# Optimization experiments

Hardware: AMD Instinct MI355X
Metric: run time of the kernel (lower is better)

## Reference

```python
import jax, jax.numpy as jnp
import numpy as np

B, D, N, M, R, C = 512, 16, 64, 32, 32, 10  # batch, divisions, feat_in, feat_map, TR-rank, categories


def setup_inputs() -> dict:
    key = jax.random.key(0)
    k1, k2, k3, k4 = jax.random.split(key, 4)
    tensor = jax.random.normal(k1, (B, D, N), dtype=jnp.float32)
    W_fm = jax.random.normal(k2, (N, M), dtype=jnp.float32) / np.sqrt(N)
    b_fm = jax.random.normal(k3, (M,), dtype=jnp.float32) * 0.01
    # one [R, M, R] tensor-ring core per (category, division)
    G = jax.random.normal(k4, (C, D, R, M, R), dtype=jnp.float32) / np.sqrt(M * R)
    return {"tensor": tensor, "W_fm": W_fm, "b_fm": b_fm, "G": G}


def reference(tensor, W_fm, b_fm, G):
    # FeatureMap: learned linear n -> m applied per division  [B, D, M]
    feat = jnp.einsum('bdn,nm->bdm', tensor, W_fm) + b_fm
    # CoreKernelTensorRing per (category, division): [B,M] x [R,M,R] -> [B,R,R]
    cores = jnp.einsum('bdm,cdimj->cdbij', feat, G)  # [C, D, B, R, R]
    # __foward_products: chained batched matmul along divisions (structural loop, D fixed)
    prod = cores[:, 0]  # [C, B, R, R]
    for d in range(1, D):
        prod = jnp.matmul(prod, cores[:, d])
    # __calculate_traces: per-sample trace, one logit per category
    logits = jnp.einsum('cbii->bc', prod)  # [B, C]
    return jax.nn.log_softmax(logits, axis=1)
```

## Files before the change

kernel.cpp:

```cpp
#include <hip/hip_runtime.h>
#include <math.h>

#define BB 512
#define DD 16
#define NN 64
#define MM 32
#define RR 32
#define CC 10
#define BBLK 16
#define ROWH 40
#define BREGH 1304

typedef _Float16 v8h __attribute__((ext_vector_type(8)));
typedef float v4f __attribute__((ext_vector_type(4)));

union H8 { unsigned int u[4]; v8h h; _Float16 e[8]; };
union H4 { unsigned int u[2]; _Float16 e[4]; };

__global__ __launch_bounds__(256) void produce_kernel(
    const float* __restrict__ tensor, const float* __restrict__ W,
    const float* __restrict__ bias,   const float* __restrict__ G,
    _Float16* __restrict__ fh,        _Float16* __restrict__ gh) {
    __shared__ __align__(16) char smem[36864];
    const int t = threadIdx.x;
    if (blockIdx.x < 1024) {
        float* ten_s = (float*)smem;
        float* W_s   = (float*)smem + 512;
        const int bd0 = blockIdx.x * 8;
        if (t < 128)
            *(float4*)(ten_s + t * 4) = *(const float4*)(tensor + bd0 * NN + t * 4);
        *(float4*)(W_s + t * 4)        = *(const float4*)(W + t * 4);
        *(float4*)(W_s + 1024 + t * 4) = *(const float4*)(W + 1024 + t * 4);
        __syncthreads();
        const int m = t & 31, bd_l = t >> 5;
        float acc = bias[m];
#pragma unroll
        for (int n = 0; n < NN; ++n) acc += ten_s[bd_l * NN + n] * W_s[n * MM + m];
        fh[(bd0 + bd_l) * MM + m] = (_Float16)acc;
    } else {
        _Float16* lg = (_Float16*)smem;
        const int pb = blockIdx.x - 1024;
        const int c  = pb >> 5;
        const int d  = (pb >> 1) & 15;
        const int hf = pb & 1;
        const float* src = G + (size_t)(c * DD + d) * 32768 + hf * 16384;
#pragma unroll
        for (int k = 0; k < 16; ++k) {
            const int f = (k * 256 + t) * 4;
            float4 v = *(const float4*)(src + f);
            const int di = f >> 10, m = (f >> 5) & 31, j = f & 31;
            H4 hv;
            hv.e[0] = (_Float16)v.x; hv.e[1] = (_Float16)v.y;
            hv.e[2] = (_Float16)v.z; hv.e[3] = (_Float16)v.w;
            *(uint2*)(lg + di * 1152 + m * 36 + j) = make_uint2(hv.u[0], hv.u[1]);
        }
        __syncthreads();
#pragma unroll
        for (int k = 0; k < 8; ++k) {
            const int idx = k * 256 + t;
            const int tl = idx >> 6, ln = idx & 63;
            const int di = tl >> 1, jh = tl & 1;
            const int q = ln >> 4, j4 = ln & 15;
            const int j = jh * 16 + j4;
            H8 o;
#pragma unroll
            for (int r = 0; r < 8; ++r)
                o.e[r] = lg[di * 1152 + (8 * q + r) * 36 + j];
            const size_t gi = ((size_t)(c * DD + d) * 64 + hf * 32 + tl) * 64 + ln;
            *(v8h*)(gh + gi * 8) = o.h;
        }
    }
}

__global__ __launch_bounds__(512, 4) void chain_kernel(
    const _Float16* __restrict__ feat_h,
    const _Float16* __restrict__ g_h,
    float* __restrict__ trout)
{
    __shared__ __align__(16) _Float16 lds[BBLK * BREGH];

    const int bid = blockIdx.x;
    const int xcd = bid & 7;
    const int idx = bid >> 3;
    int c, sub;
    if (idx < 32) { c = xcd; sub = idx; }
    else {
        const int e = idx - 32;
        if (xcd >= 2 && xcd <= 5) { c = 8; sub = (xcd - 2) * 8 + e; }
        else                      { c = 9; sub = (((xcd + 2) & 7)) * 8 + e; }
    }
    const int b0 = sub * BBLK;
    const int t    = threadIdx.x;
    const int w    = t >> 6;
    const int lane = t & 63;
    const int q    = lane >> 4;
    const int j4   = lane & 15;

    const int bA = b0 + j4;
    const size_t gc = (size_t)c * DD * 32768;

    v8h afh = *(const v8h*)(feat_h + (size_t)bA * (DD * MM) + 0 * MM + q * 8);
    v8h gf[8];
#pragma unroll
    for (int u = 0; u < 8; ++u)
        gf[u] = *(const v8h*)(g_h + gc + ((size_t)(w * 8 + u) * 64 + lane) * 8);

    v8h sb[2][2];

    for (int d = 0; d < DD; ++d) {
        __syncthreads();
        v4f av[8];
#pragma unroll
        for (int u = 0; u < 8; ++u) {
            v4f z = {0.f, 0.f, 0.f, 0.f};
            av[u] = __builtin_amdgcn_mfma_f32_16x16x32_f16(afh, gf[u], z, 0, 0, 0);
        }
        if (d < DD - 1) {
            afh = *(const v8h*)(feat_h + (size_t)bA * (DD * MM) + (d + 1) * MM + q * 8);
            const size_t gb = gc + (size_t)(d + 1) * 32768;
#pragma unroll
            for (int u = 0; u < 8; ++u)
                gf[u] = *(const v8h*)(g_h + gb + ((size_t)(w * 8 + u) * 64 + lane) * 8);
        }
#pragma unroll
        for (int jh = 0; jh < 2; ++jh)
#pragma unroll
            for (int reg = 0; reg < 4; ++reg) {
                H4 hv;
                hv.e[0] = (_Float16)av[0 + jh][reg];
                hv.e[1] = (_Float16)av[2 + jh][reg];
                hv.e[2] = (_Float16)av[4 + jh][reg];
                hv.e[3] = (_Float16)av[6 + jh][reg];
                *(uint2*)(&lds[(4 * q + reg) * BREGH + (16 * jh + j4) * ROWH + 4 * w]) =
                    make_uint2(hv.u[0], hv.u[1]);
            }
        __syncthreads();
#pragma unroll
        for (int cc = 0; cc < 2; ++cc) {
            const int bl = 2 * w + cc;
            _Float16* base = lds + bl * BREGH;
            if (d == 0) {
#pragma unroll
                for (int vt = 0; vt < 2; ++vt) {
                    H8 x;
#pragma unroll
                    for (int r = 0; r < 8; ++r)
                        x.e[r] = base[(8 * q + r) * ROWH + 16 * vt + j4];
                    sb[cc][vt] = x.h;
                }
            } else {
                v8h af2[2];
#pragma unroll
                for (int jt = 0; jt < 2; ++jt)
                    af2[jt] = *(const v8h*)(base + (16 * jt + j4) * ROWH + 8 * q);
                if (d == DD - 1) {
                    v4f z0 = {0.f, 0.f, 0.f, 0.f};
                    v4f a0 = __builtin_amdgcn_mfma_f32_16x16x32_f16(
                        af2[0], sb[cc][0], z0, 0, 0, 0);
                    v4f z1 = {0.f, 0.f, 0.f, 0.f};
                    v4f a1 = __builtin_amdgcn_mfma_f32_16x16x32_f16(
                        af2[1], sb[cc][1], z1, 0, 0, 0);
                    float ts = 0.f;
#pragma unroll
                    for (int reg = 0; reg < 4; ++reg)
                        if (j4 == 4 * q + reg) ts = a0[reg] + a1[reg];
#pragma unroll
                    for (int off = 32; off > 0; off >>= 1)
                        ts += __shfl_xor(ts, off);
                    if (lane == 0) trout[(size_t)(b0 + bl) * CC + c] = ts;
                } else {
                    v4f acc[2][2];
#pragma unroll
                    for (int jt = 0; jt < 2; ++jt)
#pragma unroll
                        for (int vt = 0; vt < 2; ++vt) {
                            v4f z = {0.f, 0.f, 0.f, 0.f};
                            acc[jt][vt] = __builtin_amdgcn_mfma_f32_16x16x32_f16(
                                af2[jt], sb[cc][vt], z, 0, 0, 0);
                        }
#pragma unroll
                    for (int jt = 0; jt < 2; ++jt)
#pragma unroll
                        for (int vt = 0; vt < 2; ++vt) {
                            H4 hv;
                            hv.e[0] = (_Float16)acc[jt][vt][0];
                            hv.e[1] = (_Float16)acc[jt][vt][1];
                            hv.e[2] = (_Float16)acc[jt][vt][2];
                            hv.e[3] = (_Float16)acc[jt][vt][3];
                            *(uint2*)(base + (16 * vt + j4) * ROWH + 16 * jt + 4 * q) =
                                make_uint2(hv.u[0], hv.u[1]);
                        }
                    __builtin_amdgcn_sched_barrier(0);
#pragma unroll
                    for (int vt = 0; vt < 2; ++vt)
                        sb[cc][vt] = *(const v8h*)(base + (16 * vt + j4) * ROWH + 8 * q);
                }
            }
        }
    }
}

__global__ __launch_bounds__(256) void lsm_kernel(
    const float* __restrict__ tr, float* __restrict__ out) {
    const int b = blockIdx.x * 256 + threadIdx.x;
    float v[CC];
    float mx = -1e30f;
#pragma unroll
    for (int c = 0; c < CC; ++c) {
        v[c] = tr[b * CC + c];
        mx = fmaxf(mx, v[c]);
    }
    float ssum = 0.f;
#pragma unroll
    for (int c = 0; c < CC; ++c) ssum += expf(v[c] - mx);
    const float ls = logf(ssum);
#pragma unroll
    for (int c = 0; c < CC; ++c) out[b * CC + c] = v[c] - mx - ls;
}

extern "C" void kernel_launch(void* const* d_in, const int* in_sizes, int n_in,
                              void* d_out, int out_size, void* d_ws, size_t ws_size,
                              hipStream_t stream) {
    const float* tensor = (const float*)d_in[0];
    const float* W      = (const float*)d_in[1];
    const float* bias   = (const float*)d_in[2];
    const float* G      = (const float*)d_in[3];
    float* out = (float*)d_out;

    const size_t FEAT = (size_t)BB * DD * MM;
    const size_t GPK  = (size_t)CC * DD * 64 * 64 * 8;
    _Float16* fh = (_Float16*)d_ws;
    _Float16* gh = fh + FEAT;
    float* trbuf = (float*)(gh + GPK);

    produce_kernel<<<1024 + 320, 256, 0, stream>>>(tensor, W, bias, G, fh, gh);
    chain_kernel<<<CC * (BB / BBLK), 512, 0, stream>>>(fh, gh, trbuf);
    lsm_kernel<<<BB / 256, 256, 0, stream>>>(trbuf, out);
}
```

Before: 114.7 us.

## Process two 16-sample batch sets per chain block to reuse loaded cores

Each chain_kernel block now handles 32 batch samples instead of 16, reusing the per-division G core fragments held in registers for two sets of feature MFMAs. This halves the number of blocks and the redundant global loads of G per category, and remaps the block-to-XCD assignment to the new grid of 160 blocks. In exchange, LDS use doubles, register pressure rises (launch bounds drop to 2 blocks per CU), and fewer blocks may leave parts of the GPU underused.

```diff
diff --git a/kernel.cpp b/kernel.cpp
--- a/kernel.cpp
+++ b/kernel.cpp
@@ -8,6 +8,7 @@
 #define RR 32
 #define CC 10
 #define BBLK 16
+#define SETS 2
 #define ROWH 40
 #define BREGH 1304
 
@@ -72,73 +73,85 @@
     }
 }
 
-__global__ __launch_bounds__(512, 4) void chain_kernel(
+__global__ __launch_bounds__(512, 2) void chain_kernel(
     const _Float16* __restrict__ feat_h,
     const _Float16* __restrict__ g_h,
     float* __restrict__ trout)
 {
-    __shared__ __align__(16) _Float16 lds[BBLK * BREGH];
+    __shared__ __align__(16) _Float16 lds[SETS * BBLK * BREGH];
 
     const int bid = blockIdx.x;
     const int xcd = bid & 7;
     const int idx = bid >> 3;
     int c, sub;
-    if (idx < 32) { c = xcd; sub = idx; }
+    if (idx < 16) { c = xcd; sub = idx; }
     else {
-        const int e = idx - 32;
-        if (xcd >= 2 && xcd <= 5) { c = 8; sub = (xcd - 2) * 8 + e; }
-        else                      { c = 9; sub = (((xcd + 2) & 7)) * 8 + e; }
-    }
-    const int b0 = sub * BBLK;
+        const int e = idx - 16;
+        c = 8 + (xcd >> 2);
+        sub = (xcd & 3) * 4 + e;
+    }
+    const int b0 = sub * (SETS * BBLK);
     const int t    = threadIdx.x;
     const int w    = t >> 6;
     const int lane = t & 63;
     const int q    = lane >> 4;
     const int j4   = lane & 15;
 
-    const int bA = b0 + j4;
     const size_t gc = (size_t)c * DD * 32768;
 
-    v8h afh = *(const v8h*)(feat_h + (size_t)bA * (DD * MM) + 0 * MM + q * 8);
+    v8h afh[2];
+#pragma unroll
+    for (int bs = 0; bs < 2; ++bs)
+        afh[bs] = *(const v8h*)(feat_h + (size_t)(b0 + 16 * bs + j4) * (DD * MM) + q * 8);
     v8h gf[8];
 #pragma unroll
     for (int u = 0; u < 8; ++u)
         gf[u] = *(const v8h*)(g_h + gc + ((size_t)(w * 8 + u) * 64 + lane) * 8);
 
-    v8h sb[2][2];
+    v8h sb[4][2];
 
     for (int d = 0; d < DD; ++d) {
         __syncthreads();
-        v4f av[8];
-#pragma unroll
-        for (int u = 0; u < 8; ++u) {
-            v4f z = {0.f, 0.f, 0.f, 0.f};
-            av[u] = __builtin_amdgcn_mfma_f32_16x16x32_f16(afh, gf[u], z, 0, 0, 0);
-        }
+        v4f av[2][8];
+#pragma unroll
+        for (int bs = 0; bs < 2; ++bs)
+#pragma unroll
+            for (int u = 0; u < 8; ++u) {
+                v4f z = {0.f, 0.f, 0.f, 0.f};
+                av[bs][u] = __builtin_amdgcn_mfma_f32_16x16x32_f16(
+                    afh[bs], gf[u], z, 0, 0, 0);
+            }
         if (d < DD - 1) {
-            afh = *(const v8h*)(feat_h + (size_t)bA * (DD * MM) + (d + 1) * MM + q * 8);
+#pragma unroll
+            for (int bs = 0; bs < 2; ++bs)
+                afh[bs] = *(const v8h*)(feat_h +
+                    (size_t)(b0 + 16 * bs + j4) * (DD * MM) + (d + 1) * MM + q * 8);
             const size_t gb = gc + (size_t)(d + 1) * 32768;
 #pragma unroll
             for (int u = 0; u < 8; ++u)
                 gf[u] = *(const v8h*)(g_h + gb + ((size_t)(w * 8 + u) * 64 + lane) * 8);
         }
 #pragma unroll
-        for (int jh = 0; jh < 2; ++jh)
-#pragma unroll
-            for (int reg = 0; reg < 4; ++reg) {
-                H4 hv;
-                hv.e[0] = (_Float16)av[0 + jh][reg];
-                hv.e[1] = (_Float16)av[2 + jh][reg];
-                hv.e[2] = (_Float16)av[4 + jh][reg];
-                hv.e[3] = (_Float16)av[6 + jh][reg];
-                *(uint2*)(&lds[(4 * q + reg) * BREGH + (16 * jh + j4) * ROWH + 4 * w]) =
-                    make_uint2(hv.u[0], hv.u[1]);
-            }
-        __syncthreads();
-#pragma unroll
-        for (int cc = 0; cc < 2; ++cc) {
-            const int bl = 2 * w + cc;
-            _Float16* base = lds + bl * BREGH;
+        for (int bs = 0; bs < 2; ++bs)
+#pragma unroll
+            for (int jh = 0; jh < 2; ++jh)
+#pragma unroll
+                for (int reg = 0; reg < 4; ++reg) {
+                    H4 hv;
+                    hv.e[0] = (_Float16)av[bs][0 + jh][reg];
+                    hv.e[1] = (_Float16)av[bs][2 + jh][reg];
+                    hv.e[2] = (_Float16)av[bs][4 + jh][reg];
+                    hv.e[3] = (_Float16)av[bs][6 + jh][reg];
+                    *(uint2*)(&lds[(bs * BBLK + 4 * q + reg) * BREGH +
+                                   (16 * jh + j4) * ROWH + 4 * w]) =
+                        make_uint2(hv.u[0], hv.u[1]);
+                }
+        __syncthreads();
+#pragma unroll
+        for (int ch = 0; ch < 4; ++ch) {
+            const int bs = ch >> 1;
+            const int bl = 2 * w + (ch & 1);
+            _Float16* base = lds + (bs * BBLK + bl) * BREGH;
             if (d == 0) {
 #pragma unroll
                 for (int vt = 0; vt < 2; ++vt) {
@@ -146,7 +159,7 @@
 #pragma unroll
                     for (int r = 0; r < 8; ++r)
                         x.e[r] = base[(8 * q + r) * ROWH + 16 * vt + j4];
-                    sb[cc][vt] = x.h;
+                    sb[ch][vt] = x.h;
                 }
             } else {
                 v8h af2[2];
@@ -156,10 +169,10 @@
                 if (d == DD - 1) {
                     v4f z0 = {0.f, 0.f, 0.f, 0.f};
                     v4f a0 = __builtin_amdgcn_mfma_f32_16x16x32_f16(
-                        af2[0], sb[cc][0], z0, 0, 0, 0);
+                        af2[0], sb[ch][0], z0, 0, 0, 0);
                     v4f z1 = {0.f, 0.f, 0.f, 0.f};
                     v4f a1 = __builtin_amdgcn_mfma_f32_16x16x32_f16(
-                        af2[1], sb[cc][1], z1, 0, 0, 0);
+                        af2[1], sb[ch][1], z1, 0, 0, 0);
                     float ts = 0.f;
 #pragma unroll
                     for (int reg = 0; reg < 4; ++reg)
@@ -167,7 +180,8 @@
 #pragma unroll
                     for (int off = 32; off > 0; off >>= 1)
                         ts += __shfl_xor(ts, off);
-                    if (lane == 0) trout[(size_t)(b0 + bl) * CC + c] = ts;
+                    if (lane == 0)
+                        trout[(size_t)(b0 + 16 * bs + bl) * CC + c] = ts;
                 } else {
                     v4f acc[2][2];
 #pragma unroll
@@ -176,7 +190,7 @@
                         for (int vt = 0; vt < 2; ++vt) {
                             v4f z = {0.f, 0.f, 0.f, 0.f};
                             acc[jt][vt] = __builtin_amdgcn_mfma_f32_16x16x32_f16(
-                                af2[jt], sb[cc][vt], z, 0, 0, 0);
+                                af2[jt], sb[ch][vt], z, 0, 0, 0);
                         }
 #pragma unroll
                     for (int jt = 0; jt < 2; ++jt)
@@ -193,7 +207,7 @@
                     __builtin_amdgcn_sched_barrier(0);
 #pragma unroll
                     for (int vt = 0; vt < 2; ++vt)
-                        sb[cc][vt] = *(const v8h*)(base + (16 * vt + j4) * ROWH + 8 * q);
+                        sb[ch][vt] = *(const v8h*)(base + (16 * vt + j4) * ROWH + 8 * q);
                 }
             }
         }
@@ -234,6 +248,6 @@
     float* trbuf = (float*)(gh + GPK);
 
     produce_kernel<<<1024 + 320, 256, 0, stream>>>(tensor, W, bias, G, fh, gh);
-    chain_kernel<<<CC * (BB / BBLK), 512, 0, stream>>>(fh, gh, trbuf);
+    chain_kernel<<<CC * (BB / (SETS * BBLK)), 512, 0, stream>>>(fh, gh, trbuf);
     lsm_kernel<<<BB / 256, 256, 0, stream>>>(trbuf, out);
 }
```

Result: no change. 117.0 us (+2.0%).
